# Optimization experiments

Hardware: AMD Instinct MI355X
Metric: run time of the kernel (lower is better)

Reference implementation:

```python
import jax, jax.numpy as jnp
import numpy as np

B = 32768
IN_F = 256
OUT_F = 256


def setup_inputs() -> dict:
    key = jax.random.key(0)
    k1, k2 = jax.random.split(key)
    x = jax.random.normal(k1, (B, IN_F, 4), dtype=jnp.float32)
    std = 1.0 / np.sqrt(4 * IN_F)
    weight = jax.random.normal(k2, (OUT_F, IN_F, 4), dtype=jnp.float32) * std
    weight = weight.at[..., 0].add(0.5)  # quaternion Xavier: bias real part
    bias = jnp.zeros((OUT_F, 4), dtype=jnp.float32)
    return {"x": x, "weight": weight, "bias": bias}


def _quat_linear(x, weight, bias):
    # x: (..., in, 4) with components (w, x, y, z); weight: (out, in, 4)
    # Hamilton product q1=W, q2=x, summed over in -> 16 structured matmuls.
    xw, xx, xy, xz = x[..., 0], x[..., 1], x[..., 2], x[..., 3]
    ww, wx, wy, wz = weight[..., 0], weight[..., 1], weight[..., 2], weight[..., 3]

    def mm(w, v):  # (out, in) x (..., in) -> (..., out)
        return jnp.einsum('oi,...i->...o', w, v)

    yw = mm(ww, xw) - mm(wx, xx) - mm(wy, xy) - mm(wz, xz)
    yx = mm(ww, xx) + mm(wx, xw) + mm(wy, xz) - mm(wz, xy)
    yy = mm(ww, xy) - mm(wx, xz) + mm(wy, xw) + mm(wz, xx)
    yz = mm(ww, xz) + mm(wx, xy) - mm(wy, xx) + mm(wz, xw)

    y = jnp.stack([yw, yx, yy, yz], axis=-1)  # (..., out, 4)
    return y + bias


def reference(x, weight, bias):
    return _quat_linear(x, weight, bias)
```

## Files before the change

### kernel.cpp

```cpp
#include <hip/hip_runtime.h>


typedef __bf16 bf16x8_t __attribute__((ext_vector_type(8)));
typedef short short8    __attribute__((ext_vector_type(8)));
typedef float f32x4     __attribute__((ext_vector_type(4)));
typedef float f32x8     __attribute__((ext_vector_type(8)));

typedef const unsigned int __attribute__((address_space(1)))* gas_uint_ptr;
typedef unsigned int __attribute__((address_space(3)))*       las_uint_ptr;

__global__ __launch_bounds__(256) void build_weff(const float* __restrict__ w,
                                                  unsigned short* __restrict__ wq) {
    int idx = blockIdx.x * 256 + threadIdx.x;
    int n = idx >> 10, k = idx & 1023;
    int o = n >> 2, r = n & 3, i = k >> 2, c = k & 3;
    int s = r ^ c;
    float v = w[o * 1024 + i * 4 + s];
    if ((0x284E >> (r * 4 + c)) & 1) v = -v;
    union { __bf16 b; unsigned short u; } cv;
    cv.b = (__bf16)v;
    wq[idx] = cv.u;
}

__global__ __launch_bounds__(256) void conv_x(const float* __restrict__ x,
                                              unsigned short* __restrict__ xb) {
    const long long c = (long long)blockIdx.x * 256 + threadIdx.x;
    const float* gp = x + c * 8;
    f32x4 lo = *(const f32x4*)gp;
    f32x4 hi = *(const f32x4*)(gp + 4);
    f32x8 f8 = __builtin_shufflevector(lo, hi, 0, 1, 2, 3, 4, 5, 6, 7);
    bf16x8_t bv = __builtin_convertvector(f8, bf16x8_t);
    union { bf16x8_t b; short8 s; } cv;
    cv.b = bv;
    *(short8*)(xb + c * 8) = cv.s;
}

__global__ __launch_bounds__(256) void qlin_gemm_bf(const unsigned short* __restrict__ Xb,
                                                    const unsigned short* __restrict__ Wq,
                                                    const float* __restrict__ bias,
                                                    float* __restrict__ out) {
    __shared__ __align__(16) unsigned short As[128 * 64];
    __shared__ __align__(16) unsigned short Bs[128 * 64];

    const int t    = threadIdx.x;
    const int w    = t >> 6;
    const int l    = t & 63;
    const int lo16 = l & 15;
    const int hi2  = l >> 4;

    const int bid  = blockIdx.x;
    const int xcd  = bid & 7;
    const int s    = bid >> 3;
    const int m0   = (xcd * 32 + (s >> 3)) * 128;
    const int n0   = (s & 7) * 128;

    const int wm   = (w & 1) * 64;
    const int wn   = (w >> 1) * 64;

    f32x4 acc[4][4] = {};

    for (int kt = 0; kt < 16; ++kt) {
        const int k0 = kt * 64;
        __syncthreads();

#pragma unroll
        for (int jj = 0; jj < 4; ++jj) {
            const int p    = jj * 256 + t;
            const int row  = p >> 3;
            const int g    = (p & 7) ^ (row & 7);
            const unsigned short* ga = Xb + (long long)(m0 + row) * 1024 + k0 + g * 8;
            const unsigned short* gb = Wq + (n0 + row) * 1024 + k0 + g * 8;
            __builtin_amdgcn_global_load_lds((gas_uint_ptr)ga,
                                             (las_uint_ptr)(As + p * 8), 16, 0, 0);
            __builtin_amdgcn_global_load_lds((gas_uint_ptr)gb,
                                             (las_uint_ptr)(Bs + p * 8), 16, 0, 0);
        }

        __syncthreads();

#pragma unroll
        for (int ks = 0; ks < 2; ++ks) {
            const int g = ks * 4 + hi2;
            short8 af[4], bf[4];
#pragma unroll
            for (int mt = 0; mt < 4; ++mt) {
                const int r = wm + mt * 16 + lo16;
                af[mt] = *(const short8*)(As + (r * 8 + (g ^ (r & 7))) * 8);
            }
#pragma unroll
            for (int nt = 0; nt < 4; ++nt) {
                const int r = wn + nt * 16 + lo16;
                bf[nt] = *(const short8*)(Bs + (r * 8 + (g ^ (r & 7))) * 8);
            }
#pragma unroll
            for (int mt = 0; mt < 4; ++mt)
#pragma unroll
                for (int nt = 0; nt < 4; ++nt)
                    acc[mt][nt] = __builtin_amdgcn_mfma_f32_16x16x32_bf16(
                        af[mt], bf[nt], acc[mt][nt], 0, 0, 0);
        }
    }

#pragma unroll
    for (int nt = 0; nt < 4; ++nt) {
        const int n  = n0 + wn + nt * 16 + lo16;
        const float bv = bias[n];
#pragma unroll
        for (int mt = 0; mt < 4; ++mt) {
            const int mb = m0 + wm + mt * 16 + hi2 * 4;
#pragma unroll
            for (int r = 0; r < 4; ++r)
                out[(long long)(mb + r) * 1024 + n] = acc[mt][nt][r] + bv;
        }
    }
}

__global__ __launch_bounds__(256) void qlin_gemm_fused(const float* __restrict__ X,
                                                       const unsigned short* __restrict__ Wq,
                                                       const float* __restrict__ bias,
                                                       float* __restrict__ out) {
    __shared__ __align__(16) unsigned short As[128 * 64];
    __shared__ __align__(16) unsigned short Bs[128 * 64];

    const int t    = threadIdx.x;
    const int w    = t >> 6;
    const int l    = t & 63;
    const int lo16 = l & 15;
    const int hi2  = l >> 4;
    const int bid  = blockIdx.x;
    const int xcd  = bid & 7;
    const int s    = bid >> 3;
    const int m0   = (xcd * 32 + (s >> 3)) * 128;
    const int n0   = (s & 7) * 128;
    const int wm   = (w & 1) * 64;
    const int wn   = (w >> 1) * 64;

    f32x4 acc[4][4] = {};

    for (int kt = 0; kt < 16; ++kt) {
        const int k0 = kt * 64;
        __syncthreads();
#pragma unroll
        for (int jj = 0; jj < 4; ++jj) {
            const int p    = jj * 256 + t;
            const int row  = p >> 3;
            const int g    = (p & 7) ^ (row & 7);
            const unsigned short* gp = Wq + (n0 + row) * 1024 + k0 + g * 8;
            __builtin_amdgcn_global_load_lds((gas_uint_ptr)gp,
                                             (las_uint_ptr)(Bs + p * 8), 16, 0, 0);
        }
#pragma unroll
        for (int jj = 0; jj < 4; ++jj) {
            const int c    = jj * 256 + t;
            const int row  = c >> 3;
            const int g    = c & 7;
            const float* gp = X + (long long)(m0 + row) * 1024 + k0 + g * 8;
            f32x4 lo = *(const f32x4*)gp;
            f32x4 hi = *(const f32x4*)(gp + 4);
            f32x8 f8 = __builtin_shufflevector(lo, hi, 0, 1, 2, 3, 4, 5, 6, 7);
            bf16x8_t bv = __builtin_convertvector(f8, bf16x8_t);
            union { bf16x8_t b; short8 s; } cv;
            cv.b = bv;
            const int p = row * 8 + (g ^ (row & 7));
            *(short8*)(As + p * 8) = cv.s;
        }
        __syncthreads();
#pragma unroll
        for (int ks = 0; ks < 2; ++ks) {
            const int g = ks * 4 + hi2;
            short8 af[4], bf[4];
#pragma unroll
            for (int mt = 0; mt < 4; ++mt) {
                const int r = wm + mt * 16 + lo16;
                af[mt] = *(const short8*)(As + (r * 8 + (g ^ (r & 7))) * 8);
            }
#pragma unroll
            for (int nt = 0; nt < 4; ++nt) {
                const int r = wn + nt * 16 + lo16;
                bf[nt] = *(const short8*)(Bs + (r * 8 + (g ^ (r & 7))) * 8);
            }
#pragma unroll
            for (int mt = 0; mt < 4; ++mt)
#pragma unroll
                for (int nt = 0; nt < 4; ++nt)
                    acc[mt][nt] = __builtin_amdgcn_mfma_f32_16x16x32_bf16(
                        af[mt], bf[nt], acc[mt][nt], 0, 0, 0);
        }
    }

#pragma unroll
    for (int nt = 0; nt < 4; ++nt) {
        const int n  = n0 + wn + nt * 16 + lo16;
        const float bv = bias[n];
#pragma unroll
        for (int mt = 0; mt < 4; ++mt) {
            const int mb = m0 + wm + mt * 16 + hi2 * 4;
#pragma unroll
            for (int r = 0; r < 4; ++r)
                out[(long long)(mb + r) * 1024 + n] = acc[mt][nt][r] + bv;
        }
    }
}

extern "C" void kernel_launch(void* const* d_in, const int* in_sizes, int n_in,
                              void* d_out, int out_size, void* d_ws, size_t ws_size,
                              hipStream_t stream) {
    const float* x  = (const float*)d_in[0];
    const float* wt = (const float*)d_in[1];
    const float* bs = (const float*)d_in[2];
    float* out = (float*)d_out;

    unsigned short* wq = (unsigned short*)d_ws;
    const size_t WQ_BYTES = 1024ull * 1024 * 2;
    const size_t XB_BYTES = 32768ull * 1024 * 2;

    build_weff<<<4096, 256, 0, stream>>>(wt, wq);

    if (ws_size >= WQ_BYTES + XB_BYTES) {
        unsigned short* xb = (unsigned short*)((char*)d_ws + WQ_BYTES);
        conv_x<<<16384, 256, 0, stream>>>(x, xb);
        qlin_gemm_bf<<<2048, 256, 0, stream>>>(xb, wq, bs, out);
    } else {
        qlin_gemm_fused<<<2048, 256, 0, stream>>>(x, wq, bs, out);
    }

    (void)in_sizes; (void)n_in; (void)out_size;
}
```

Measured before the change: 313.7 us.

## Replace bf16 GEMM with 256x256-tile double-buffered eight-phase pipelined kernel

Replaces the 128x128-tile, single-buffered GEMM with a 512-thread kernel that computes 256x256 output tiles. A/B tiles are double-buffered in LDS, and each k-step is split into eight phases that interleave global_load_lds staging of the next tiles with MFMA work, using explicit barriers, waitcnts and setprio. The aim is to hide global-load latency and raise reuse of each loaded tile. In exchange it uses 128KB of LDS and many more accumulator registers, and the hand-placed waitcnt counts must exactly match the loads in flight.

```diff
diff --git a/kernel.cpp b/kernel.cpp
--- a/kernel.cpp
+++ b/kernel.cpp
@@ -35,12 +35,13 @@
     *(short8*)(xb + c * 8) = cv.s;
 }
 
-__global__ __launch_bounds__(256) void qlin_gemm_bf(const unsigned short* __restrict__ Xb,
-                                                    const unsigned short* __restrict__ Wq,
-                                                    const float* __restrict__ bias,
-                                                    float* __restrict__ out) {
-    __shared__ __align__(16) unsigned short As[128 * 64];
-    __shared__ __align__(16) unsigned short Bs[128 * 64];
+__global__ __launch_bounds__(512, 2) void qlin_gemm_8ph(
+        const unsigned short* __restrict__ Xb,
+        const unsigned short* __restrict__ Wq,
+        const float* __restrict__ bias,
+        float* __restrict__ out) {
+    __shared__ __align__(16) unsigned short As[2][2][128 * 64];
+    __shared__ __align__(16) unsigned short Bs[2][2][128 * 64];
 
     const int t    = threadIdx.x;
     const int w    = t >> 6;
@@ -48,65 +49,128 @@
     const int lo16 = l & 15;
     const int hi2  = l >> 4;
 
-    const int bid  = blockIdx.x;
-    const int xcd  = bid & 7;
-    const int s    = bid >> 3;
-    const int m0   = (xcd * 32 + (s >> 3)) * 128;
-    const int n0   = (s & 7) * 128;
-
-    const int wm   = (w & 1) * 64;
-    const int wn   = (w >> 1) * 64;
-
-    f32x4 acc[4][4] = {};
-
-    for (int kt = 0; kt < 16; ++kt) {
-        const int k0 = kt * 64;
-        __syncthreads();
-
-#pragma unroll
-        for (int jj = 0; jj < 4; ++jj) {
-            const int p    = jj * 256 + t;
-            const int row  = p >> 3;
-            const int g    = (p & 7) ^ (row & 7);
-            const unsigned short* ga = Xb + (long long)(m0 + row) * 1024 + k0 + g * 8;
-            const unsigned short* gb = Wq + (n0 + row) * 1024 + k0 + g * 8;
-            __builtin_amdgcn_global_load_lds((gas_uint_ptr)ga,
-                                             (las_uint_ptr)(As + p * 8), 16, 0, 0);
-            __builtin_amdgcn_global_load_lds((gas_uint_ptr)gb,
-                                             (las_uint_ptr)(Bs + p * 8), 16, 0, 0);
-        }
-
-        __syncthreads();
-
-#pragma unroll
-        for (int ks = 0; ks < 2; ++ks) {
-            const int g = ks * 4 + hi2;
-            short8 af[4], bf[4];
-#pragma unroll
-            for (int mt = 0; mt < 4; ++mt) {
-                const int r = wm + mt * 16 + lo16;
-                af[mt] = *(const short8*)(As + (r * 8 + (g ^ (r & 7))) * 8);
-            }
-#pragma unroll
-            for (int nt = 0; nt < 4; ++nt) {
-                const int r = wn + nt * 16 + lo16;
-                bf[nt] = *(const short8*)(Bs + (r * 8 + (g ^ (r & 7))) * 8);
-            }
-#pragma unroll
-            for (int mt = 0; mt < 4; ++mt)
-#pragma unroll
-                for (int nt = 0; nt < 4; ++nt)
-                    acc[mt][nt] = __builtin_amdgcn_mfma_f32_16x16x32_bf16(
-                        af[mt], bf[nt], acc[mt][nt], 0, 0, 0);
-        }
-    }
+    const int bid     = blockIdx.x;
+    const int xcd     = bid & 7;
+    const int logical = xcd * 64 + (bid >> 3);
+    const int m0      = (logical >> 2) * 256;
+    const int n0      = (logical & 3) * 256;
+
+    const int wm  = (w >> 2) * 128;
+    const int wn  = (w & 3) * 64;
+    const int hA  = wm >> 7;
+    const int hB  = wn >> 7;
+    const int rbB = wn & 64;
+
+    f32x4 acc[8][4] = {};
+    short8 af[2][2];
+    short8 bf[4][2];
+
+    const int sw    = lo16 & 7;
+    const int slot0 = hi2 ^ sw;
+    const int slot1 = (4 + hi2) ^ sw;
+
+#define STAGE_A(KT, H) do {                                                     \
+        const int kk_ = ((KT) & 15) * 64;                                       \
+        _Pragma("unroll")                                                       \
+        for (int jj = 0; jj < 2; ++jj) {                                        \
+            const int idx_ = jj * 512 + t;                                      \
+            const int row_ = idx_ >> 3;                                         \
+            const int g_   = (idx_ & 7) ^ (row_ & 7);                           \
+            const unsigned short* ga_ =                                         \
+                Xb + (long long)(m0 + (H) * 128 + row_) * 1024 + kk_ + g_ * 8;  \
+            __builtin_amdgcn_global_load_lds((gas_uint_ptr)ga_,                 \
+                (las_uint_ptr)(&As[(KT) & 1][(H)][idx_ * 8]), 16, 0, 0);        \
+        }                                                                       \
+    } while (0)
+
+#define STAGE_B(KT, H) do {                                                     \
+        const int kk_ = ((KT) & 15) * 64;                                       \
+        _Pragma("unroll")                                                       \
+        for (int jj = 0; jj < 2; ++jj) {                                        \
+            const int idx_ = jj * 512 + t;                                      \
+            const int row_ = idx_ >> 3;                                         \
+            const int g_   = (idx_ & 7) ^ (row_ & 7);                           \
+            const unsigned short* gb_ =                                         \
+                Wq + (n0 + (H) * 128 + row_) * 1024 + kk_ + g_ * 8;             \
+            __builtin_amdgcn_global_load_lds((gas_uint_ptr)gb_,                 \
+                (las_uint_ptr)(&Bs[(KT) & 1][(H)][idx_ * 8]), 16, 0, 0);        \
+        }                                                                       \
+    } while (0)
+
+#define READ_BF(PAR) do {                                                       \
+        _Pragma("unroll")                                                       \
+        for (int nt = 0; nt < 4; ++nt) {                                        \
+            const int rl_ = rbB + nt * 16 + lo16;                               \
+            bf[nt][0] = *(const short8*)(&Bs[(PAR)][hB][rl_ * 64 + slot0 * 8]); \
+            bf[nt][1] = *(const short8*)(&Bs[(PAR)][hB][rl_ * 64 + slot1 * 8]); \
+        }                                                                       \
+    } while (0)
+
+#define READ_AF(PAR, MTB) do {                                                  \
+        _Pragma("unroll")                                                       \
+        for (int mi = 0; mi < 2; ++mi) {                                        \
+            const int rl_ = ((MTB) + mi) * 16 + lo16;                           \
+            af[mi][0] = *(const short8*)(&As[(PAR)][hA][rl_ * 64 + slot0 * 8]); \
+            af[mi][1] = *(const short8*)(&As[(PAR)][hA][rl_ * 64 + slot1 * 8]); \
+        }                                                                       \
+    } while (0)
+
+#define MFMA_Q(MTB) do {                                                        \
+        _Pragma("unroll")                                                       \
+        for (int mi = 0; mi < 2; ++mi)                                          \
+            _Pragma("unroll")                                                   \
+            for (int nt = 0; nt < 4; ++nt) {                                    \
+                acc[(MTB) + mi][nt] = __builtin_amdgcn_mfma_f32_16x16x32_bf16(  \
+                    af[mi][0], bf[nt][0], acc[(MTB) + mi][nt], 0, 0, 0);        \
+                acc[(MTB) + mi][nt] = __builtin_amdgcn_mfma_f32_16x16x32_bf16(  \
+                    af[mi][1], bf[nt][1], acc[(MTB) + mi][nt], 0, 0, 0);        \
+            }                                                                   \
+    } while (0)
+
+#define PHASE(PAR, MTB, RDB, ENDW, STAGE_STMT) do {                             \
+        if (RDB) READ_BF(PAR);                                                  \
+        READ_AF(PAR, MTB);                                                      \
+        STAGE_STMT;                                                             \
+        asm volatile("s_barrier" ::: "memory");                                 \
+        asm volatile("s_waitcnt lgkmcnt(0)" ::: "memory");                      \
+        __builtin_amdgcn_s_setprio(1);                                          \
+        MFMA_Q(MTB);                                                            \
+        __builtin_amdgcn_s_setprio(0);                                          \
+        if (ENDW) asm volatile("s_waitcnt vmcnt(4)" ::: "memory");              \
+        asm volatile("s_barrier" ::: "memory");                                 \
+    } while (0)
+
+    STAGE_B(0, 0); STAGE_B(0, 1);
+    STAGE_A(0, 0); STAGE_A(0, 1);
+    STAGE_B(1, 0); STAGE_B(1, 1);
+    asm volatile("s_waitcnt vmcnt(4)" ::: "memory");
+    asm volatile("s_barrier" ::: "memory");
+
+    for (int i = 0; i < 8; ++i) {
+        const int kt1 = 2 * i + 1;
+        PHASE(0, 0, true,  false, STAGE_A(kt1, 0));
+        PHASE(0, 2, false, false, STAGE_A(kt1, 1));
+        PHASE(0, 4, false, false, STAGE_B(kt1 + 1, 0));
+        PHASE(0, 6, false, true,  STAGE_B(kt1 + 1, 1));
+        PHASE(1, 0, true,  false, STAGE_A(kt1 + 1, 0));
+        PHASE(1, 2, false, false, STAGE_A(kt1 + 1, 1));
+        PHASE(1, 4, false, false, STAGE_B(kt1 + 2, 0));
+        PHASE(1, 6, false, true,  STAGE_B(kt1 + 2, 1));
+    }
+
+#undef STAGE_A
+#undef STAGE_B
+#undef READ_BF
+#undef READ_AF
+#undef MFMA_Q
+#undef PHASE
 
 #pragma unroll
     for (int nt = 0; nt < 4; ++nt) {
         const int n  = n0 + wn + nt * 16 + lo16;
         const float bv = bias[n];
 #pragma unroll
-        for (int mt = 0; mt < 4; ++mt) {
+        for (int mt = 0; mt < 8; ++mt) {
             const int mb = m0 + wm + mt * 16 + hi2 * 4;
 #pragma unroll
             for (int r = 0; r < 4; ++r)
@@ -219,7 +283,7 @@
     if (ws_size >= WQ_BYTES + XB_BYTES) {
         unsigned short* xb = (unsigned short*)((char*)d_ws + WQ_BYTES);
         conv_x<<<16384, 256, 0, stream>>>(x, xb);
-        qlin_gemm_bf<<<2048, 256, 0, stream>>>(xb, wq, bs, out);
+        qlin_gemm_8ph<<<512, 512, 0, stream>>>(xb, wq, bs, out);
     } else {
         qlin_gemm_fused<<<2048, 256, 0, stream>>>(x, wq, bs, out);
     }
```

New measurement: 305.5 us. -2.6%, faster.
